# Optimization experiments

Hardware: AMD Instinct MI355X
Metric: run time of the kernel (lower is better)

The kernel has to match this reference:

```python
import jax, jax.numpy as jnp
import numpy as np


def setup_inputs() -> dict:
    key = jax.random.key(0)
    ks = jax.random.split(key, 8)
    B = 65536
    scale = lambda fan_in: 1.0 / np.sqrt(fan_in)
    return {
        "x": jax.random.normal(ks[0], (B, 784), dtype=jnp.float32),
        "w0": jax.random.normal(ks[1], (124, 784), dtype=jnp.float32) * scale(784),
        "w1": jax.random.normal(ks[2], (32, 124), dtype=jnp.float32) * scale(124),
        "w3": jax.random.normal(ks[3], (22, 32), dtype=jnp.float32) * scale(32),
        "b3": jax.random.normal(ks[4], (22,), dtype=jnp.float32) * scale(32),
        "w5": jax.random.normal(ks[5], (21, 22), dtype=jnp.float32) * scale(22),
        "b5": jax.random.normal(ks[6], (21,), dtype=jnp.float32) * scale(22),
        "w7": jax.random.normal(ks[7], (10, 21), dtype=jnp.float32) * scale(21),
    }


def reference(x, w0, w1, w3, b3, w5, b5, w7):
    # x: [B, 784]; PyTorch Linear: y = x @ W.T (+ b)
    h = x @ w0.T                       # [B, 124] (no bias, no activation)
    h = jax.nn.relu(h @ w1.T)          # [B, 32]
    h = jax.nn.relu(h @ w3.T + b3)     # [B, 22]
    h = jax.nn.relu(h @ w5.T + b5)     # [B, 21]
    logits = h @ w7.T                  # [B, 10]
    return jax.nn.log_softmax(logits, axis=1)
```

## Files before the change

kernel.cpp:

```cpp
#include <hip/hip_runtime.h>
#include <hip/hip_fp16.h>

typedef _Float16 half8 __attribute__((ext_vector_type(8)));
typedef __fp16 cvt2_t __attribute__((ext_vector_type(2)));
typedef float f32x4 __attribute__((ext_vector_type(4)));

#define W0F_UNITS (13 * 1024)
#define W1F_OFF   (W0F_UNITS * 16)
#define W1F_UNITS 512
#define SW_OFF    (W1F_OFF + W1F_UNITS * 16)

#define L_H0   0
#define L_H1   8192
#define L_H3   0
#define L_H5   3200
#define L_OS   6400
#define LDS_SZ 10240

__global__ void prep_weights(const float* __restrict__ w0,
                             const float* __restrict__ w1,
                             const float* __restrict__ w3,
                             const float* __restrict__ b3,
                             const float* __restrict__ w5,
                             const float* __restrict__ b5,
                             const float* __restrict__ w7,
                             char* __restrict__ ws) {
  int tid = blockIdx.x * 256 + threadIdx.x;
  if (tid < W0F_UNITS) {
    int t  = tid >> 10;
    int kf = (tid >> 9) & 1;
    int nf = (tid >> 6) & 7;
    int l  = tid & 63;
    int n  = nf * 16 + (l & 15);
    int k0 = t * 64 + kf * 32 + (l >> 4) * 8;
    alignas(16) __half h[8];
#pragma unroll
    for (int e = 0; e < 8; e++) {
      int k = k0 + e;
      h[e] = __float2half((n < 124 && k < 784) ? w0[n * 784 + k] : 0.f);
    }
    *(uint4*)(ws + tid * 16) = *(const uint4*)h;
    return;
  }
  int r = tid - W0F_UNITS;
  if (r < W1F_UNITS) {
    int kf = r >> 7;
    int nf = (r >> 6) & 1;
    int l  = r & 63;
    int n  = nf * 16 + (l & 15);
    int k0 = kf * 32 + (l >> 4) * 8;
    alignas(16) __half h[8];
#pragma unroll
    for (int e = 0; e < 8; e++) {
      int k = k0 + e;
      h[e] = __float2half((k < 124) ? w1[n * 124 + k] : 0.f);
    }
    *(uint4*)(ws + W1F_OFF + r * 16) = *(const uint4*)h;
    return;
  }
  r -= W1F_UNITS;
  float* sw = (float*)(ws + SW_OFF);
  if (r < 704) { sw[r] = w3[r]; return; }
  r -= 704;
  if (r < 504) {
    int n = r / 24, k = r % 24;
    sw[704 + r] = (k < 22) ? w5[n * 22 + k] : 0.f;
    return;
  }
  r -= 504;
  if (r < 240) {
    int n = r / 24, k = r % 24;
    sw[1208 + r] = (k < 21) ? w7[n * 21 + k] : 0.f;
    return;
  }
  r -= 240;
  if (r < 24) { sw[1448 + r] = (r < 22) ? b3[r] : 0.f; return; }
  r -= 24;
  if (r < 24) { sw[1472 + r] = (r < 21) ? b5[r] : 0.f; return; }
}

__device__ __forceinline__ half8 cvt8(const f32x4& a, const f32x4& b) {
  cvt2_t p0 = __builtin_amdgcn_cvt_pkrtz(a[0], a[1]);
  cvt2_t p1 = __builtin_amdgcn_cvt_pkrtz(a[2], a[3]);
  cvt2_t p2 = __builtin_amdgcn_cvt_pkrtz(b[0], b[1]);
  cvt2_t p3 = __builtin_amdgcn_cvt_pkrtz(b[2], b[3]);
  uint4 u;
  u.x = __builtin_bit_cast(unsigned, p0);
  u.y = __builtin_bit_cast(unsigned, p1);
  u.z = __builtin_bit_cast(unsigned, p2);
  u.w = __builtin_bit_cast(unsigned, p3);
  return __builtin_bit_cast(half8, u);
}

__global__ __launch_bounds__(64, 2) void fused_mlp(
    const float* __restrict__ x, const char* __restrict__ ws,
    float* __restrict__ out) {
  __shared__ alignas(16) char sm[LDS_SZ];
  const int l  = threadIdx.x;
  const int lr = l & 15;
  const int lg = l >> 4;
  const size_t row0 = (size_t)blockIdx.x * 32;

  const float* xb0 = x + (row0 + lr) * 784;
  const float* xb1 = xb0 + 16 * 784;

  f32x4 acc[2][8];
#pragma unroll
  for (int mf = 0; mf < 2; mf++)
#pragma unroll
    for (int nf = 0; nf < 8; nf++) acc[mf][nf] = f32x4{0.f, 0.f, 0.f, 0.f};

  const uint4* wf = (const uint4*)ws;

  f32x4 xP[2][2][2], xQ[2][2][2];
  half8 bfr[2][8];

#define XLOAD(T, B, G)                                                         \
  {                                                                            \
    _Pragma("unroll") for (int mf = 0; mf < 2; mf++)                           \
        _Pragma("unroll") for (int kf = 0; kf < 2; kf++) {                     \
      const float* p = (mf ? xb1 : xb0) + (T) * 64 + kf * 32 + lg * 8;         \
      if (!(G) || (kf == 0 && lg < 2)) {                                       \
        B[mf][kf][0] = *(const f32x4*)p;                                       \
        B[mf][kf][1] = *(const f32x4*)(p + 4);                                 \
      } else {                                                                 \
        B[mf][kf][0] = f32x4{0.f, 0.f, 0.f, 0.f};                              \
        B[mf][kf][1] = f32x4{0.f, 0.f, 0.f, 0.f};                              \
      }                                                                        \
    }                                                                          \
  }

#define BF(T)                                                                  \
  _Pragma("unroll") for (int kf = 0; kf < 2; kf++)                             \
      _Pragma("unroll") for (int nf = 0; nf < 8; nf++)                         \
          bfr[kf][nf] = __builtin_bit_cast(                                    \
              half8, wf[(T) * 1024 + kf * 512 + nf * 64 + l]);

#define BODY(B)                                                                \
  {                                                                            \
    half8 af[2][2];                                                            \
    _Pragma("unroll") for (int mf = 0; mf < 2; mf++)                           \
        _Pragma("unroll") for (int kf = 0; kf < 2; kf++)                       \
            af[mf][kf] = cvt8(B[mf][kf][0], B[mf][kf][1]);                     \
    _Pragma("unroll") for (int kf = 0; kf < 2; kf++)                           \
        _Pragma("unroll") for (int mf = 0; mf < 2; mf++)                       \
            _Pragma("unroll") for (int nf = 0; nf < 8; nf++)                   \
                acc[mf][nf] = __builtin_amdgcn_mfma_f32_16x16x32_f16(          \
                    af[mf][kf], bfr[kf][nf], acc[mf][nf], 0, 0, 0);            \
  }

  XLOAD(0, xP, 0)
  BF(0)
  XLOAD(1, xQ, 0)

  BODY(xP) BF(1)  XLOAD(2, xP, 0)
  BODY(xQ) BF(2)  XLOAD(3, xQ, 0)
  BODY(xP) BF(3)  XLOAD(4, xP, 0)
  BODY(xQ) BF(4)  XLOAD(5, xQ, 0)
  BODY(xP) BF(5)  XLOAD(6, xP, 0)
  BODY(xQ) BF(6)  XLOAD(7, xQ, 0)
  BODY(xP) BF(7)  XLOAD(8, xP, 0)
  BODY(xQ) BF(8)  XLOAD(9, xQ, 0)
  BODY(xP) BF(9)  XLOAD(10, xP, 0)
  BODY(xQ) BF(10) XLOAD(11, xQ, 0)
  BODY(xP) BF(11) XLOAD(12, xP, 1)
  BODY(xQ) BF(12)
  BODY(xP)

  half8 b1[4][2];
  {
    const uint4* w1f = (const uint4*)(ws + W1F_OFF);
#pragma unroll
    for (int kf = 0; kf < 4; kf++)
#pragma unroll
      for (int nf = 0; nf < 2; nf++)
        b1[kf][nf] = __builtin_bit_cast(half8, w1f[kf * 128 + nf * 64 + l]);
  }

#pragma unroll
  for (int mf = 0; mf < 2; mf++)
#pragma unroll
    for (int nf = 0; nf < 8; nf++)
#pragma unroll
      for (int q = 0; q < 4; q++) {
        int rr = mf * 16 + lg * 4 + q;
        int cc = nf * 16 + lr;
        *(__half*)(sm + L_H0 + rr * 256 + ((2 * cc) ^ ((rr & 7) << 4))) =
            __float2half(acc[mf][nf][q]);
      }
  __syncthreads();

  f32x4 acc1[2][2];
#pragma unroll
  for (int mf = 0; mf < 2; mf++) {
    acc1[mf][0] = f32x4{0.f, 0.f, 0.f, 0.f};
    acc1[mf][1] = f32x4{0.f, 0.f, 0.f, 0.f};
  }
#pragma unroll
  for (int kf = 0; kf < 4; kf++) {
    half8 a1[2];
#pragma unroll
    for (int mf = 0; mf < 2; mf++) {
      int rr = mf * 16 + lr;
      int cb = kf * 64 + lg * 16;
      a1[mf] = *(const half8*)(sm + L_H0 + rr * 256 + (cb ^ ((rr & 7) << 4)));
    }
#pragma unroll
    for (int mf = 0; mf < 2; mf++)
#pragma unroll
      for (int nf = 0; nf < 2; nf++)
        acc1[mf][nf] = __builtin_amdgcn_mfma_f32_16x16x32_f16(
            a1[mf], b1[kf][nf], acc1[mf][nf], 0, 0, 0);
  }
#pragma unroll
  for (int mf = 0; mf < 2; mf++)
#pragma unroll
    for (int nf = 0; nf < 2; nf++)
#pragma unroll
      for (int q = 0; q < 4; q++) {
        int rr = mf * 16 + lg * 4 + q;
        int cc = nf * 16 + lr;
        float v = fmaxf(acc1[mf][nf][q], 0.f);
        *(__half*)(sm + L_H1 + rr * 64 + ((2 * cc) ^ ((rr & 3) << 4))) =
            __float2half(v);
      }
  __syncthreads();

  const int r = l & 31;
  const int j = l >> 5;
  float h1v[32];
#pragma unroll
  for (int cb = 0; cb < 4; cb++) {
    half8 v = *(const half8*)(sm + L_H1 + r * 64 + ((cb * 16) ^ ((r & 3) << 4)));
#pragma unroll
    for (int e = 0; e < 8; e++) h1v[cb * 8 + e] = (float)v[e];
  }
  const float* w3g = (const float*)(ws + SW_OFF);
  const float* w5g = (const float*)(ws + SW_OFF + 2816);
  const float* w7g = (const float*)(ws + SW_OFF + 4832);
  const float* b3g = (const float*)(ws + SW_OFF + 5792);
  const float* b5g = (const float*)(ws + SW_OFF + 5888);
  float* h3l = (float*)(sm + L_H3);
  float* h5l = (float*)(sm + L_H5);

#pragma unroll
  for (int i = 0; i < 11; i++) {
    int n = j + 2 * i;
    float s = b3g[n];
    const float4* wrow = (const float4*)(w3g + n * 32);
#pragma unroll
    for (int kk = 0; kk < 8; kk++) {
      float4 wv = wrow[kk];
      s += h1v[4 * kk] * wv.x + h1v[4 * kk + 1] * wv.y +
           h1v[4 * kk + 2] * wv.z + h1v[4 * kk + 3] * wv.w;
    }
    h3l[r * 25 + n] = fmaxf(s, 0.f);
  }
  __syncthreads();
  float h3v[24];
#pragma unroll
  for (int k = 0; k < 24; k++) h3v[k] = (k < 22) ? h3l[r * 25 + k] : 0.f;
#pragma unroll
  for (int i = 0; i < 11; i++) {
    int n = j + 2 * i;
    if (n < 21) {
      float s = b5g[n];
      const float4* wrow = (const float4*)(w5g + n * 24);
#pragma unroll
      for (int kk = 0; kk < 6; kk++) {
        float4 wv = wrow[kk];
        s += h3v[4 * kk] * wv.x + h3v[4 * kk + 1] * wv.y +
             h3v[4 * kk + 2] * wv.z + h3v[4 * kk + 3] * wv.w;
      }
      h5l[r * 25 + n] = fmaxf(s, 0.f);
    }
  }
  __syncthreads();
  if (j == 0) {
    float h5v[24];
#pragma unroll
    for (int k = 0; k < 24; k++) h5v[k] = (k < 21) ? h5l[r * 25 + k] : 0.f;
    float lgt[10];
    float mx = -3.4e38f;
#pragma unroll
    for (int n = 0; n < 10; n++) {
      float s = 0.f;
      const float4* wrow = (const float4*)(w7g + n * 24);
#pragma unroll
      for (int kk = 0; kk < 6; kk++) {
        float4 wv = wrow[kk];
        s += h5v[4 * kk] * wv.x + h5v[4 * kk + 1] * wv.y +
             h5v[4 * kk + 2] * wv.z + h5v[4 * kk + 3] * wv.w;
      }
      lgt[n] = s;
      mx = fmaxf(mx, s);
    }
    float se = 0.f;
#pragma unroll
    for (int n = 0; n < 10; n++) se += __expf(lgt[n] - mx);
    const float lse = mx + __logf(se);
    float* os = (float*)(sm + L_OS);
#pragma unroll
    for (int n = 0; n < 10; n++) os[r * 10 + n] = lgt[n] - lse;
  }
  __syncthreads();
  {
    const float* os = (const float*)(sm + L_OS);
#pragma unroll
    for (int i = 0; i < 5; i++) out[row0 * 10 + i * 64 + l] = os[i * 64 + l];
  }
}

extern "C" void kernel_launch(void* const* d_in, const int* in_sizes, int n_in,
                              void* d_out, int out_size, void* d_ws, size_t ws_size,
                              hipStream_t stream) {
  const float* x  = (const float*)d_in[0];
  const float* w0 = (const float*)d_in[1];
  const float* w1 = (const float*)d_in[2];
  const float* w3 = (const float*)d_in[3];
  const float* b3 = (const float*)d_in[4];
  const float* w5 = (const float*)d_in[5];
  const float* b5 = (const float*)d_in[6];
  const float* w7 = (const float*)d_in[7];
  float* out = (float*)d_out;
  char* ws = (char*)d_ws;

  const int prep_threads = W0F_UNITS + W1F_UNITS + 704 + 504 + 240 + 24 + 24;
  prep_weights<<<(prep_threads + 255) / 256, 256, 0, stream>>>(w0, w1, w3, b3,
                                                               w5, b5, w7, ws);
  fused_mlp<<<65536 / 32, 64, 0, stream>>>(x, ws, out);
}
```

Before: 57.62 us.

## Restructure layer-0 K loop into 128-wide stages with interleaved weight prefetch

```diff
diff --git a/kernel.cpp b/kernel.cpp
--- a/kernel.cpp
+++ b/kernel.cpp
@@ -100,6 +100,7 @@
   const int lr = l & 15;
   const int lg = l >> 4;
   const size_t row0 = (size_t)blockIdx.x * 32;
+  const uint4* wf = (const uint4*)ws;
 
   const float* xb0 = x + (row0 + lr) * 784;
   const float* xb1 = xb0 + 16 * 784;
@@ -110,62 +111,74 @@
 #pragma unroll
     for (int nf = 0; nf < 8; nf++) acc[mf][nf] = f32x4{0.f, 0.f, 0.f, 0.f};
 
-  const uint4* wf = (const uint4*)ws;
-
-  f32x4 xP[2][2][2], xQ[2][2][2];
+  f32x4 xr[2][4][2];
+  half8 afr[2][4];
   half8 bfr[2][8];
 
-#define XLOAD(T, B, G)                                                         \
+#define XL(T, G)                                                               \
   {                                                                            \
     _Pragma("unroll") for (int mf = 0; mf < 2; mf++)                           \
-        _Pragma("unroll") for (int kf = 0; kf < 2; kf++) {                     \
-      const float* p = (mf ? xb1 : xb0) + (T) * 64 + kf * 32 + lg * 8;         \
-      if (!(G) || (kf == 0 && lg < 2)) {                                       \
-        B[mf][kf][0] = *(const f32x4*)p;                                       \
-        B[mf][kf][1] = *(const f32x4*)(p + 4);                                 \
-      } else {                                                                 \
-        B[mf][kf][0] = f32x4{0.f, 0.f, 0.f, 0.f};                              \
-        B[mf][kf][1] = f32x4{0.f, 0.f, 0.f, 0.f};                              \
-      }                                                                        \
+        _Pragma("unroll") for (int kf = 0; kf < 4; kf++)                       \
+            _Pragma("unroll") for (int h = 0; h < 2; h++) {                    \
+      const float* p =                                                         \
+          (mf ? xb1 : xb0) + (T) * 128 + kf * 32 + lg * 8 + h * 4;             \
+      if (!(G) || (kf == 0 && lg < 2))                                         \
+        xr[mf][kf][h] = *(const f32x4*)p;                                      \
+      else                                                                     \
+        xr[mf][kf][h] = f32x4{0.f, 0.f, 0.f, 0.f};                             \
     }                                                                          \
   }
 
-#define BF(T)                                                                  \
-  _Pragma("unroll") for (int kf = 0; kf < 2; kf++)                             \
-      _Pragma("unroll") for (int nf = 0; nf < 8; nf++)                         \
-          bfr[kf][nf] = __builtin_bit_cast(                                    \
-              half8, wf[(T) * 1024 + kf * 512 + nf * 64 + l]);
-
-#define BODY(B)                                                                \
-  {                                                                            \
-    half8 af[2][2];                                                            \
+#define CVALL()                                                                \
+  {                                                                            \
     _Pragma("unroll") for (int mf = 0; mf < 2; mf++)                           \
-        _Pragma("unroll") for (int kf = 0; kf < 2; kf++)                       \
-            af[mf][kf] = cvt8(B[mf][kf][0], B[mf][kf][1]);                     \
-    _Pragma("unroll") for (int kf = 0; kf < 2; kf++)                           \
-        _Pragma("unroll") for (int mf = 0; mf < 2; mf++)                       \
-            _Pragma("unroll") for (int nf = 0; nf < 8; nf++)                   \
-                acc[mf][nf] = __builtin_amdgcn_mfma_f32_16x16x32_f16(          \
-                    af[mf][kf], bfr[kf][nf], acc[mf][nf], 0, 0, 0);            \
-  }
-
-  XLOAD(0, xP, 0)
-  BF(0)
-  XLOAD(1, xQ, 0)
-
-  BODY(xP) BF(1)  XLOAD(2, xP, 0)
-  BODY(xQ) BF(2)  XLOAD(3, xQ, 0)
-  BODY(xP) BF(3)  XLOAD(4, xP, 0)
-  BODY(xQ) BF(4)  XLOAD(5, xQ, 0)
-  BODY(xP) BF(5)  XLOAD(6, xP, 0)
-  BODY(xQ) BF(6)  XLOAD(7, xQ, 0)
-  BODY(xP) BF(7)  XLOAD(8, xP, 0)
-  BODY(xQ) BF(8)  XLOAD(9, xQ, 0)
-  BODY(xP) BF(9)  XLOAD(10, xP, 0)
-  BODY(xQ) BF(10) XLOAD(11, xQ, 0)
-  BODY(xP) BF(11) XLOAD(12, xP, 1)
-  BODY(xQ) BF(12)
-  BODY(xP)
+        _Pragma("unroll") for (int kf = 0; kf < 4; kf++)                       \
+            afr[mf][kf] = cvt8(xr[mf][kf][0], xr[mf][kf][1]);                  \
+  }
+
+#define BFL(P, G)                                                              \
+  {                                                                            \
+    _Pragma("unroll") for (int nf = 0; nf < 8; nf++)                           \
+      bfr[P][nf] = __builtin_bit_cast(                                         \
+          half8, wf[((G) >> 1) * 1024 + ((G) & 1) * 512 + nf * 64 + l]);       \
+  }
+
+#define MFK(KF, P)                                                             \
+  {                                                                            \
+    _Pragma("unroll") for (int nf = 0; nf < 8; nf++) {                         \
+      acc[0][nf] = __builtin_amdgcn_mfma_f32_16x16x32_f16(                     \
+          afr[0][KF], bfr[P][nf], acc[0][nf], 0, 0, 0);                        \
+      acc[1][nf] = __builtin_amdgcn_mfma_f32_16x16x32_f16(                     \
+          afr[1][KF], bfr[P][nf], acc[1][nf], 0, 0, 0);                        \
+    }                                                                          \
+  }
+
+#define BODY(T, GN)                                                            \
+  {                                                                            \
+    CVALL()                                                                    \
+    XL((T) + 1, GN)                                                            \
+    MFK(0, 0)                                                                  \
+    BFL(0, (T) * 4 + 2)                                                        \
+    MFK(1, 1)                                                                  \
+    BFL(1, (T) * 4 + 3)                                                        \
+    MFK(2, 0)                                                                  \
+    BFL(0, ((T) + 1) * 4 + 0)                                                  \
+    MFK(3, 1)                                                                  \
+    BFL(1, ((T) + 1) * 4 + 1)                                                  \
+  }
+
+  XL(0, 0)
+  BFL(0, 0)
+  BFL(1, 1)
+
+  BODY(0, 0)
+  BODY(1, 0)
+  BODY(2, 0)
+  BODY(3, 0)
+  BODY(4, 0)
+  BODY(5, 1)
+  CVALL()
+  MFK(0, 0)
 
   half8 b1[4][2];
   {
```

Result: slower. 60.99 us (+5.9%).
